# Optimization experiments

Hardware: AMD Instinct MI355X
Metric: run time of the kernel (lower is better)

## Reference

```python
import jax, jax.numpy as jnp
import numpy as np

N, D, H, B, K = 65536, 64, 128, 16, 16
EPS = 0.0

def setup_inputs() -> dict:
    key = jax.random.key(0)
    ks = jax.random.split(key, 5)
    x = jax.random.normal(ks[0], (N, D), dtype=jnp.float32)
    pos = jax.random.normal(ks[1], (N, 3), dtype=jnp.float32)
    batch = (jnp.arange(N, dtype=jnp.int32) // (N // B)).astype(jnp.int32)
    W1 = jax.random.normal(ks[2], (D, H), dtype=jnp.float32) * (1.0 / np.sqrt(D))
    b1 = jnp.zeros((H,), dtype=jnp.float32)
    W2 = jax.random.normal(ks[3], (H, D), dtype=jnp.float32) * (1.0 / np.sqrt(H))
    b2 = jnp.zeros((D,), dtype=jnp.float32)
    return {"x": x, "pos": pos, "batch": batch, "W1": W1, "b1": b1, "W2": W2, "b2": b2}

def reference(x, pos, batch, W1, b1, W2, b2):
    # batch is assumed contiguous with B equal segments of n nodes each
    n = N // B
    pos_s = pos.reshape(B, n, 3)
    x_s = x.reshape(B, n, D)
    # pairwise squared distances per segment via gram trick: [B, n, n]
    sq = jnp.sum(pos_s * pos_s, axis=-1)
    d2 = sq[:, :, None] + sq[:, None, :] - 2.0 * jnp.einsum('bic,bjc->bij', pos_s, pos_s)
    # exclude self-loops (loop=False in knn_graph)
    d2 = jnp.where(jnp.eye(n, dtype=bool)[None], jnp.inf, d2)
    # k nearest neighbors per node: indices [B, n, K]
    _, idx = jax.lax.top_k(-d2, K)
    # GIN sum aggregation: gather neighbor features and sum over K
    nb = x_s[jnp.arange(B)[:, None, None], idx]        # [B, n, K, D]
    agg = nb.sum(axis=2).reshape(N, D)                  # [N, D]
    h = (1.0 + EPS) * x + agg
    h = jax.nn.relu(h @ W1 + b1)
    out = h @ W2 + b2
    return out
```

## Files before the change

### kernel.cpp

```cpp
#include <hip/hip_runtime.h>
#include <math.h>

#define DIM  64
#define HID  128
#define KNN  16
#define SEG  1024
#define TSZ  128
#define CAP  14

typedef unsigned long long u64;
typedef __attribute__((ext_vector_type(8))) short short8;
typedef __attribute__((ext_vector_type(4))) float f32x4;
#define INF_BITS 0x7F800000u

__device__ __forceinline__ unsigned short bf16_rn(float f) {
    unsigned u = __float_as_uint(f);
    unsigned r = u + 0x7FFFu + ((u >> 16) & 1u);
    return (unsigned short)(r >> 16);
}
__device__ __forceinline__ float bf16_f32(unsigned short b) {
    return __uint_as_float(((unsigned)b) << 16);
}

__device__ __forceinline__ void ins16(float (&bd)[KNN], int (&bi)[KNN],
                                      float d, int g) {
    float cd = d; int ci = g;
    #pragma unroll
    for (int i = 0; i < KNN; ++i) {
        bool lt = cd < bd[i];
        float dl = lt ? cd : bd[i];
        float dh = lt ? bd[i] : cd;
        int   il = lt ? ci : bi[i];
        int   ih = lt ? bi[i] : ci;
        bd[i] = dl; bi[i] = il; cd = dh; ci = ih;
    }
}

__device__ __forceinline__ void drain_buf(const u64* bufe, int tid,
        float (&bd)[KNN], int (&bi)[KNN], int& cnt,
        unsigned* thrU, int l) {
    for (int t = 0; t < CAP; ++t) {
        if (__ballot(t < cnt) == 0ull) break;
        u64 e = bufe[t * 256 + tid];
        float d = __uint_as_float((unsigned)e);
        int   g = (int)(e >> 32);
        if ((t < cnt) && (d < bd[KNN - 1])) ins16(bd, bi, d, g);
    }
    cnt = 0;
    atomicMin(&thrU[l], __float_as_uint(bd[KNN - 1]));
}

struct f2 { float a, b; };
__device__ __forceinline__ f2 f2mul(f2 x, float s) {
    #pragma clang fp contract(off)
    f2 r; r.a = x.a * s; r.b = x.b * s; return r;
}
__device__ __forceinline__ f2 f2add(f2 x, f2 y) {
    #pragma clang fp contract(off)
    f2 r; r.a = x.a + y.a; r.b = x.b + y.b; return r;
}
__device__ __forceinline__ f2 f2adds(f2 x, float s) {
    #pragma clang fp contract(off)
    f2 r; r.a = s + x.a; r.b = s + x.b; return r;
}
__device__ __forceinline__ f2 f2sub(f2 x, f2 y) {
    #pragma clang fp contract(off)
    f2 r; r.a = x.a - y.a; r.b = x.b - y.b; return r;
}
__device__ __forceinline__ f2 d2pair(f2 Px, f2 Py, f2 Pz, f2 Ps,
                                     float qx, float qy, float qz, float qs) {
    f2 dot = f2add(f2add(f2mul(Px, qx), f2mul(Py, qy)), f2mul(Pz, qz));
    return f2sub(f2adds(Ps, qs), f2mul(dot, 2.0f));
}

template<bool CHECK>
__device__ __forceinline__ void knn_scan(
    const float* __restrict__ pos, int bbase, int segbase, int qlocal, int l,
    float qx, float qy, float qz, float qs,
    float* tx, float* ty, float* tz, float* ts,
    u64* bufe, unsigned* thrU, volatile unsigned* thrv, int tid,
    float (&bd)[KNN], int (&bi)[KNN])
{
    #pragma clang fp contract(off)
    int cnt = 0;

    #pragma unroll
    for (int m = 0; m < 2; ++m) {
        int t = (m << 6) + l;
        int g = (bbase + segbase + t) * 3;
        float ax = pos[g], ay = pos[g + 1], az = pos[g + 2];
        tx[t] = ax; ty[t] = ay; tz[t] = az;
        ts[t] = (ax * ax + ay * ay) + az * az;
    }

    __syncthreads();

    #pragma unroll
    for (int k = 0; k < KNN; ++k) { bd[k] = INFINITY; bi[k] = 0x7FFFFFFF; }
    for (int jj = 0; jj < KNN; ++jj) {
        float ax = tx[jj], ay = ty[jj], az = tz[jj], as = ts[jj];
        float dot = (ax * qx + ay * qy) + az * qz;
        float d2  = (qs + as) - 2.0f * dot;
        int cj = segbase + jj;
        if (cj == qlocal) d2 = INFINITY;
        ins16(bd, bi, d2, cj);
    }
    atomicMin(&thrU[l], __float_as_uint(bd[KNN - 1]));

    int jstart = KNN;
    for (int tb = 0; tb < SEG; tb += TSZ) {
        if (tb > 0) {
            #pragma unroll
            for (int m = 0; m < 2; ++m) {
                int t = (m << 6) + l;
                int g = (bbase + segbase + tb + t) * 3;
                float ax = pos[g], ay = pos[g + 1], az = pos[g + 2];
                tx[t] = ax; ty[t] = ay; tz[t] = az;
                ts[t] = (ax * ax + ay * ay) + az * az;
            }
        }
        for (int j = jstart; j < TSZ; j += 8) {
            float tl = __uint_as_float(thrv[l]);
            float4 X0 = *(const float4*)(tx + j);
            float4 X1 = *(const float4*)(tx + j + 4);
            float4 Y0 = *(const float4*)(ty + j);
            float4 Y1 = *(const float4*)(ty + j + 4);
            float4 Z0 = *(const float4*)(tz + j);
            float4 Z1 = *(const float4*)(tz + j + 4);
            float4 S0 = *(const float4*)(ts + j);
            float4 S1 = *(const float4*)(ts + j + 4);
            const int c0 = segbase + tb + j;

            f2 dA = d2pair({X0.x, X0.y}, {Y0.x, Y0.y}, {Z0.x, Z0.y}, {S0.x, S0.y},
                           qx, qy, qz, qs);
            f2 dB = d2pair({X0.z, X0.w}, {Y0.z, Y0.w}, {Z0.z, Z0.w}, {S0.z, S0.w},
                           qx, qy, qz, qs);
            f2 dC = d2pair({X1.x, X1.y}, {Y1.x, Y1.y}, {Z1.x, Z1.y}, {S1.x, S1.y},
                           qx, qy, qz, qs);
            f2 dD = d2pair({X1.z, X1.w}, {Y1.z, Y1.w}, {Z1.z, Z1.w}, {S1.z, S1.w},
                           qx, qy, qz, qs);
            if (CHECK) {
                int s = qlocal - c0;
                if (s == 0) dA.a = INFINITY;
                if (s == 1) dA.b = INFINITY;
                if (s == 2) dB.a = INFINITY;
                if (s == 3) dB.b = INFINITY;
                if (s == 4) dC.a = INFINITY;
                if (s == 5) dC.b = INFINITY;
                if (s == 6) dD.a = INFINITY;
                if (s == 7) dD.b = INFINITY;
            }

            if (dA.a <= tl) { bufe[cnt * 256 + tid] =
                ((u64)(unsigned)(c0 + 0) << 32) | __float_as_uint(dA.a); ++cnt; }
            if (dA.b <= tl) { bufe[cnt * 256 + tid] =
                ((u64)(unsigned)(c0 + 1) << 32) | __float_as_uint(dA.b); ++cnt; }
            if (dB.a <= tl) { bufe[cnt * 256 + tid] =
                ((u64)(unsigned)(c0 + 2) << 32) | __float_as_uint(dB.a); ++cnt; }
            if (dB.b <= tl) { bufe[cnt * 256 + tid] =
                ((u64)(unsigned)(c0 + 3) << 32) | __float_as_uint(dB.b); ++cnt; }
            if (dC.a <= tl) { bufe[cnt * 256 + tid] =
                ((u64)(unsigned)(c0 + 4) << 32) | __float_as_uint(dC.a); ++cnt; }
            if (dC.b <= tl) { bufe[cnt * 256 + tid] =
                ((u64)(unsigned)(c0 + 5) << 32) | __float_as_uint(dC.b); ++cnt; }
            if (dD.a <= tl) { bufe[cnt * 256 + tid] =
                ((u64)(unsigned)(c0 + 6) << 32) | __float_as_uint(dD.a); ++cnt; }
            if (dD.b <= tl) { bufe[cnt * 256 + tid] =
                ((u64)(unsigned)(c0 + 7) << 32) | __float_as_uint(dD.b); ++cnt; }

            if (__ballot(cnt >= CAP - 8) != 0ull)
                drain_buf(bufe, tid, bd, bi, cnt, thrU, l);
        }
        jstart = 0;
    }
    drain_buf(bufe, tid, bd, bi, cnt, thrU, l);
}

__global__ __launch_bounds__(256, 4) void knn_agg(
    const float* __restrict__ x, const float* __restrict__ pos,
    float* __restrict__ agg_out)
{
    __shared__ u64 smem[4640];

    const int tid = threadIdx.x;
    const int w   = tid >> 6;
    const int l   = tid & 63;

    const int qb     = blockIdx.x;
    const int batch  = qb >> 6;
    const int bbase  = batch << 12;
    const int qlocal = ((qb & 63) << 6) + l;
    const int qglob  = bbase + qlocal;

    float* tilef = (float*)smem;
    float* tx = tilef + w * 512;
    float* ty = tx + TSZ;
    float* tz = tx + 2 * TSZ;
    float* ts = tx + 3 * TSZ;
    unsigned* thrU = (unsigned*)(tilef + 2048);
    u64* bufe = smem + 1056;

    if (tid < 64) thrU[tid] = INF_BITS;

    float qx, qy, qz, qs;
    {
        #pragma clang fp contract(off)
        qx = pos[3 * qglob + 0];
        qy = pos[3 * qglob + 1];
        qz = pos[3 * qglob + 2];
        qs = (qx * qx + qy * qy) + qz * qz;
    }

    float bd[KNN]; int bi[KNN];
    const int segbase = w << 10;
    const int wself   = (qb & 63) >> 4;
    if (w == wself)
        knn_scan<true >(pos, bbase, segbase, qlocal, l, qx, qy, qz, qs,
                        tx, ty, tz, ts, bufe, thrU, thrU, tid, bd, bi);
    else
        knn_scan<false>(pos, bbase, segbase, qlocal, l, qx, qy, qz, qs,
                        tx, ty, tz, ts, bufe, thrU, thrU, tid, bd, bi);

    __syncthreads();

    float* md  = (float*)smem;
    int*  midx = (int*)(smem + 2048);
    #pragma unroll
    for (int k = 0; k < KNN; ++k) {
        int slot = (w << 4) + k;
        md[slot * 64 + l]   = bd[k];
        midx[slot * 64 + l] = bi[k];
    }
    __syncthreads();

    if (tid < 64) {
        float bd2[KNN]; int bi2[KNN];
        #pragma unroll
        for (int k = 0; k < KNN; ++k) {
            bd2[k] = md[k * 64 + tid];
            bi2[k] = midx[k * 64 + tid];
        }
        for (int c = KNN; c < 64; ++c) {
            float d = md[c * 64 + tid];
            int   g = midx[c * 64 + tid];
            if (d < bd2[KNN - 1]) ins16(bd2, bi2, d, g);
        }
        int* mi2 = (int*)smem;
        #pragma unroll
        for (int k = 0; k < KNN; ++k) mi2[k * 64 + tid] = bi2[k];
    }
    __syncthreads();

    {
        const int* mi2 = (const int*)smem;
        const int r  = tid >> 2;
        const int p  = tid & 3;
        const int q  = (qb << 6) + r;
        const int cb = p << 4;

        int idxs[KNN];
        #pragma unroll
        for (int k = 0; k < KNN; ++k) idxs[k] = mi2[k * 64 + r];

        float4 a0 = *(const float4*)(x + (size_t)q * DIM + cb + 0);
        float4 a1 = *(const float4*)(x + (size_t)q * DIM + cb + 4);
        float4 a2 = *(const float4*)(x + (size_t)q * DIM + cb + 8);
        float4 a3 = *(const float4*)(x + (size_t)q * DIM + cb + 12);

        #pragma unroll 4
        for (int k = 0; k < KNN; ++k) {
            const float* nr = x + (size_t)(bbase + idxs[k]) * DIM + cb;
            float4 v0 = *(const float4*)(nr + 0);
            float4 v1 = *(const float4*)(nr + 4);
            float4 v2 = *(const float4*)(nr + 8);
            float4 v3 = *(const float4*)(nr + 12);
            a0.x += v0.x; a0.y += v0.y; a0.z += v0.z; a0.w += v0.w;
            a1.x += v1.x; a1.y += v1.y; a1.z += v1.z; a1.w += v1.w;
            a2.x += v2.x; a2.y += v2.y; a2.z += v2.z; a2.w += v2.w;
            a3.x += v3.x; a3.y += v3.y; a3.z += v3.z; a3.w += v3.w;
        }

        float* o = agg_out + (size_t)q * DIM + cb;
        *(float4*)(o + 0)  = a0;
        *(float4*)(o + 4)  = a1;
        *(float4*)(o + 8)  = a2;
        *(float4*)(o + 12) = a3;
    }
}

__global__ void prep_bf16(const float* __restrict__ W1,
                          const float* __restrict__ W2,
                          unsigned short* __restrict__ ws) {
    int e = blockIdx.x * 256 + threadIdx.x;
    if (e < 8192) {
        int n = e >> 6, k = e & 63;
        float v = W1[k * HID + n];
        unsigned short h = bf16_rn(v);
        ws[e] = h;
        ws[8192 + e] = bf16_rn(v - bf16_f32(h));
    } else {
        int f = e - 8192;
        int n = f >> 7, k = f & 127;
        float v = W2[k * DIM + n];
        unsigned short h = bf16_rn(v);
        ws[16384 + f] = h;
        ws[24576 + f] = bf16_rn(v - bf16_f32(h));
    }
}

__global__ __launch_bounds__(256, 2) void mlp_mfma(
    const unsigned short* __restrict__ ws,
    const float* __restrict__ b1, const float* __restrict__ b2,
    float* __restrict__ io)
{
    __shared__ unsigned short hh[64 * 136];
    __shared__ unsigned short hl[64 * 136];

    const int tid  = threadIdx.x;
    const int w    = tid >> 6;
    const int lane = tid & 63;
    const int quad = lane >> 4;
    const int col  = lane & 15;
    const int rowbase = blockIdx.x * 64 + w * 16;

    const unsigned short* w1h = ws;
    const unsigned short* w1l = ws + 8192;
    const unsigned short* w2h = ws + 16384;
    const unsigned short* w2l = ws + 24576;

    short8 ah[2], al[2];
    #pragma unroll
    for (int ks = 0; ks < 2; ++ks) {
        const float* xr = io + (size_t)(rowbase + col) * DIM + ks * 32 + quad * 8;
        float4 v0 = *(const float4*)(xr);
        float4 v1 = *(const float4*)(xr + 4);
        float xv[8] = {v0.x, v0.y, v0.z, v0.w, v1.x, v1.y, v1.z, v1.w};
        #pragma unroll
        for (int j = 0; j < 8; ++j) {
            unsigned short hb = bf16_rn(xv[j]);
            ah[ks][j] = (short)hb;
            al[ks][j] = (short)bf16_rn(xv[j] - bf16_f32(hb));
        }
    }

    f32x4 acc1[8];
    #pragma unroll
    for (int t = 0; t < 8; ++t) acc1[t] = (f32x4){0.f, 0.f, 0.f, 0.f};

    #pragma unroll
    for (int t = 0; t < 8; ++t) {
        #pragma unroll
        for (int ks = 0; ks < 2; ++ks) {
            const int off = (t * 16 + col) * 64 + ks * 32 + quad * 8;
            short8 bh = *(const short8*)(w1h + off);
            short8 bl = *(const short8*)(w1l + off);
            acc1[t] = __builtin_amdgcn_mfma_f32_16x16x32_bf16(ah[ks], bh, acc1[t], 0, 0, 0);
            acc1[t] = __builtin_amdgcn_mfma_f32_16x16x32_bf16(al[ks], bh, acc1[t], 0, 0, 0);
            acc1[t] = __builtin_amdgcn_mfma_f32_16x16x32_bf16(ah[ks], bl, acc1[t], 0, 0, 0);
        }
    }

    #pragma unroll
    for (int t = 0; t < 8; ++t) {
        float bv = b1[t * 16 + col];
        #pragma unroll
        for (int r = 0; r < 4; ++r) {
            float h = fmaxf(acc1[t][r] + bv, 0.0f);
            unsigned short hb = bf16_rn(h);
            unsigned short lb = bf16_rn(h - bf16_f32(hb));
            int rowL = w * 16 + quad * 4 + r;
            hh[rowL * 136 + t * 16 + col] = hb;
            hl[rowL * 136 + t * 16 + col] = lb;
        }
    }
    __syncthreads();

    short8 a2h[4], a2l[4];
    #pragma unroll
    for (int ks = 0; ks < 4; ++ks) {
        const int off = (w * 16 + col) * 136 + ks * 32 + quad * 8;
        a2h[ks] = *(const short8*)(hh + off);
        a2l[ks] = *(const short8*)(hl + off);
    }

    f32x4 acc2[4];
    #pragma unroll
    for (int t = 0; t < 4; ++t) acc2[t] = (f32x4){0.f, 0.f, 0.f, 0.f};

    #pragma unroll
    for (int t = 0; t < 4; ++t) {
        #pragma unroll
        for (int ks = 0; ks < 4; ++ks) {
            const int off = (t * 16 + col) * 128 + ks * 32 + quad * 8;
            short8 bh = *(const short8*)(w2h + off);
            short8 bl = *(const short8*)(w2l + off);
            acc2[t] = __builtin_amdgcn_mfma_f32_16x16x32_bf16(a2h[ks], bh, acc2[t], 0, 0, 0);
            acc2[t] = __builtin_amdgcn_mfma_f32_16x16x32_bf16(a2l[ks], bh, acc2[t], 0, 0, 0);
            acc2[t] = __builtin_amdgcn_mfma_f32_16x16x32_bf16(a2h[ks], bl, acc2[t], 0, 0, 0);
        }
    }

    #pragma unroll
    for (int t = 0; t < 4; ++t) {
        float bv = b2[t * 16 + col];
        #pragma unroll
        for (int r = 0; r < 4; ++r) {
            io[(size_t)(rowbase + quad * 4 + r) * DIM + t * 16 + col] =
                acc2[t][r] + bv;
        }
    }
}

__global__ void prep_f32(const float* __restrict__ W1, float* __restrict__ w1t) {
    int e = blockIdx.x * 256 + threadIdx.x;
    int k = e >> 7, j = e & 127;
    w1t[j * 64 + k] = W1[e];
}

__global__ __launch_bounds__(256, 2) void mlp_valu(
    const float* __restrict__ w1t, const float* __restrict__ b1,
    const float* __restrict__ W2, const float* __restrict__ b2,
    float* __restrict__ io)
{
    __shared__ float hlds[128 * 65];
    const int tid  = threadIdx.x;
    const int r    = tid & 127;
    const int half = tid >> 7;
    const int row  = blockIdx.x * 128 + r;

    float xv[DIM];
    {
        const float4* xr = (const float4*)(io + (size_t)row * DIM);
        #pragma unroll
        for (int i = 0; i < 16; ++i) {
            float4 v = xr[i];
            xv[4*i] = v.x; xv[4*i+1] = v.y; xv[4*i+2] = v.z; xv[4*i+3] = v.w;
        }
    }
    float acc[DIM];
    #pragma unroll
    for (int c = 0; c < DIM; ++c) acc[c] = 0.0f;

    const int jb = half << 6;
    for (int jj = 0; jj < 64; ++jj) {
        const int j = jb + jj;
        const float* w1 = w1t + j * DIM;
        float s0 = 0.f, s1 = 0.f, s2 = 0.f, s3 = 0.f;
        #pragma unroll
        for (int c = 0; c < DIM; c += 4) {
            s0 = fmaf(w1[c + 0], xv[c + 0], s0);
            s1 = fmaf(w1[c + 1], xv[c + 1], s1);
            s2 = fmaf(w1[c + 2], xv[c + 2], s2);
            s3 = fmaf(w1[c + 3], xv[c + 3], s3);
        }
        float h = fmaxf((s0 + s1) + (s2 + s3) + b1[j], 0.0f);
        const float* w2 = W2 + j * DIM;
        #pragma unroll
        for (int c = 0; c < DIM; ++c) acc[c] = fmaf(h, w2[c], acc[c]);
    }

    if (half == 0) {
        #pragma unroll
        for (int c = 0; c < DIM; ++c) hlds[r * 65 + c] = acc[c];
    }
    __syncthreads();
    if (half == 1) {
        float* o = io + (size_t)row * DIM;
        #pragma unroll
        for (int c = 0; c < DIM; c += 4) {
            float4 r4;
            r4.x = acc[c + 0] + hlds[r * 65 + c + 0] + b2[c + 0];
            r4.y = acc[c + 1] + hlds[r * 65 + c + 1] + b2[c + 1];
            r4.z = acc[c + 2] + hlds[r * 65 + c + 2] + b2[c + 2];
            r4.w = acc[c + 3] + hlds[r * 65 + c + 3] + b2[c + 3];
            *(float4*)(o + c) = r4;
        }
    }
}

extern "C" void kernel_launch(void* const* d_in, const int* in_sizes, int n_in,
                              void* d_out, int out_size, void* d_ws, size_t ws_size,
                              hipStream_t stream) {
    (void)in_sizes; (void)n_in; (void)out_size;
    const float* x   = (const float*)d_in[0];
    const float* pos = (const float*)d_in[1];
    const float* W1  = (const float*)d_in[3];
    const float* b1  = (const float*)d_in[4];
    const float* W2  = (const float*)d_in[5];
    const float* b2  = (const float*)d_in[6];
    float* out = (float*)d_out;

    if (ws_size >= 65536) {
        prep_bf16<<<dim3(64), dim3(256), 0, stream>>>(W1, W2, (unsigned short*)d_ws);
        knn_agg<<<dim3(1024), dim3(256), 0, stream>>>(x, pos, out);
        mlp_mfma<<<dim3(1024), dim3(256), 0, stream>>>(
            (const unsigned short*)d_ws, b1, b2, out);
    } else {
        prep_f32<<<dim3(32), dim3(256), 0, stream>>>(W1, (float*)d_ws);
        knn_agg<<<dim3(1024), dim3(256), 0, stream>>>(x, pos, out);
        mlp_valu<<<dim3(512), dim3(256), 0, stream>>>(
            (const float*)d_ws, b1, W2, b2, out);
    }
}
```

Baseline: 357.6 us.

## Compute kNN distances with split-bf16 MFMA filtering and exact fp32 reselection

Replaces the per-thread VALU distance scan and per-lane top-16 insertion with MFMA-based distance tiles, using a hi/lo bf16 split to approximate the fp32 values. The approximate distances are filtered against a per-query threshold into shared-memory candidate lists. The lists are pruned periodically, and an exact fp32 recomputation then picks the final 16 neighbours. This trades the VALU-heavy dense scan for matrix-core throughput, at the cost of list-management atomics. There is a correctness risk if candidates overflow the list cap or fall outside the 0.01 slack margin. The fp32 MLP fallback path is also removed.

```diff
diff --git a/kernel.cpp b/kernel.cpp
--- a/kernel.cpp
+++ b/kernel.cpp
@@ -1,17 +1,17 @@
 #include <hip/hip_runtime.h>
 #include <math.h>
 
-#define DIM  64
-#define HID  128
-#define KNN  16
-#define SEG  1024
-#define TSZ  128
-#define CAP  14
+#define DIM    64
+#define HID    128
+#define KNN    16
+#define CHUNK  512
+#define LCAP   64
+#define LSTR   65
+#define EPS2   0.01f
 
 typedef unsigned long long u64;
 typedef __attribute__((ext_vector_type(8))) short short8;
 typedef __attribute__((ext_vector_type(4))) float f32x4;
-#define INF_BITS 0x7F800000u
 
 __device__ __forceinline__ unsigned short bf16_rn(float f) {
     unsigned u = __float_as_uint(f);
@@ -22,237 +22,216 @@
     return __uint_as_float(((unsigned)b) << 16);
 }
 
-__device__ __forceinline__ void ins16(float (&bd)[KNN], int (&bi)[KNN],
-                                      float d, int g) {
-    float cd = d; int ci = g;
-    #pragma unroll
-    for (int i = 0; i < KNN; ++i) {
-        bool lt = cd < bd[i];
-        float dl = lt ? cd : bd[i];
-        float dh = lt ? bd[i] : cd;
-        int   il = lt ? ci : bi[i];
-        int   ih = lt ? bi[i] : ci;
-        bd[i] = dl; bi[i] = il; cd = dh; ci = ih;
-    }
-}
-
-__device__ __forceinline__ void drain_buf(const u64* bufe, int tid,
-        float (&bd)[KNN], int (&bi)[KNN], int& cnt,
-        unsigned* thrU, int l) {
-    for (int t = 0; t < CAP; ++t) {
-        if (__ballot(t < cnt) == 0ull) break;
-        u64 e = bufe[t * 256 + tid];
-        float d = __uint_as_float((unsigned)e);
-        int   g = (int)(e >> 32);
-        if ((t < cnt) && (d < bd[KNN - 1])) ins16(bd, bi, d, g);
-    }
-    cnt = 0;
-    atomicMin(&thrU[l], __float_as_uint(bd[KNN - 1]));
-}
-
-struct f2 { float a, b; };
-__device__ __forceinline__ f2 f2mul(f2 x, float s) {
+__device__ __forceinline__ u64 pack_key(float d, unsigned idx) {
+    unsigned u = __float_as_uint(d);
+    unsigned m = u ^ ((unsigned)(((int)u) >> 31) | 0x80000000u);
+    return ((u64)m << 32) | idx;
+}
+
+__device__ __forceinline__ void ins16f(float (&b)[16], float d) {
+    float c = d;
+    #pragma unroll
+    for (int i = 0; i < 16; ++i) {
+        float lo = fminf(c, b[i]);
+        float hi = fmaxf(c, b[i]);
+        b[i] = lo; c = hi;
+    }
+}
+
+__device__ __forceinline__ void ins16k(u64 (&b)[16], u64 key) {
+    u64 c = key;
+    #pragma unroll
+    for (int i = 0; i < 16; ++i) {
+        bool lt = c < b[i];
+        u64 lo = lt ? c : b[i];
+        u64 hi = lt ? b[i] : c;
+        b[i] = lo; c = hi;
+    }
+}
+
+__device__ void exact_select(const float* __restrict__ pos, int bbase, int qloc,
+                             const u64* __restrict__ L, int n,
+                             int* __restrict__ out_idx, int qi) {
     #pragma clang fp contract(off)
-    f2 r; r.a = x.a * s; r.b = x.b * s; return r;
-}
-__device__ __forceinline__ f2 f2add(f2 x, f2 y) {
-    #pragma clang fp contract(off)
-    f2 r; r.a = x.a + y.a; r.b = x.b + y.b; return r;
-}
-__device__ __forceinline__ f2 f2adds(f2 x, float s) {
-    #pragma clang fp contract(off)
-    f2 r; r.a = s + x.a; r.b = s + x.b; return r;
-}
-__device__ __forceinline__ f2 f2sub(f2 x, f2 y) {
-    #pragma clang fp contract(off)
-    f2 r; r.a = x.a - y.a; r.b = x.b - y.b; return r;
-}
-__device__ __forceinline__ f2 d2pair(f2 Px, f2 Py, f2 Pz, f2 Ps,
-                                     float qx, float qy, float qz, float qs) {
-    f2 dot = f2add(f2add(f2mul(Px, qx), f2mul(Py, qy)), f2mul(Pz, qz));
-    return f2sub(f2adds(Ps, qs), f2mul(dot, 2.0f));
-}
-
-template<bool CHECK>
-__device__ __forceinline__ void knn_scan(
-    const float* __restrict__ pos, int bbase, int segbase, int qlocal, int l,
-    float qx, float qy, float qz, float qs,
-    float* tx, float* ty, float* tz, float* ts,
-    u64* bufe, unsigned* thrU, volatile unsigned* thrv, int tid,
-    float (&bd)[KNN], int (&bi)[KNN])
-{
-    #pragma clang fp contract(off)
-    int cnt = 0;
-
-    #pragma unroll
-    for (int m = 0; m < 2; ++m) {
-        int t = (m << 6) + l;
-        int g = (bbase + segbase + t) * 3;
-        float ax = pos[g], ay = pos[g + 1], az = pos[g + 2];
-        tx[t] = ax; ty[t] = ay; tz[t] = az;
-        ts[t] = (ax * ax + ay * ay) + az * az;
-    }
-
-    __syncthreads();
-
-    #pragma unroll
-    for (int k = 0; k < KNN; ++k) { bd[k] = INFINITY; bi[k] = 0x7FFFFFFF; }
-    for (int jj = 0; jj < KNN; ++jj) {
-        float ax = tx[jj], ay = ty[jj], az = tz[jj], as = ts[jj];
-        float dot = (ax * qx + ay * qy) + az * qz;
-        float d2  = (qs + as) - 2.0f * dot;
-        int cj = segbase + jj;
-        if (cj == qlocal) d2 = INFINITY;
-        ins16(bd, bi, d2, cj);
-    }
-    atomicMin(&thrU[l], __float_as_uint(bd[KNN - 1]));
-
-    int jstart = KNN;
-    for (int tb = 0; tb < SEG; tb += TSZ) {
-        if (tb > 0) {
-            #pragma unroll
-            for (int m = 0; m < 2; ++m) {
-                int t = (m << 6) + l;
-                int g = (bbase + segbase + tb + t) * 3;
-                float ax = pos[g], ay = pos[g + 1], az = pos[g + 2];
-                tx[t] = ax; ty[t] = ay; tz[t] = az;
-                ts[t] = (ax * ax + ay * ay) + az * az;
-            }
-        }
-        for (int j = jstart; j < TSZ; j += 8) {
-            float tl = __uint_as_float(thrv[l]);
-            float4 X0 = *(const float4*)(tx + j);
-            float4 X1 = *(const float4*)(tx + j + 4);
-            float4 Y0 = *(const float4*)(ty + j);
-            float4 Y1 = *(const float4*)(ty + j + 4);
-            float4 Z0 = *(const float4*)(tz + j);
-            float4 Z1 = *(const float4*)(tz + j + 4);
-            float4 S0 = *(const float4*)(ts + j);
-            float4 S1 = *(const float4*)(ts + j + 4);
-            const int c0 = segbase + tb + j;
-
-            f2 dA = d2pair({X0.x, X0.y}, {Y0.x, Y0.y}, {Z0.x, Z0.y}, {S0.x, S0.y},
-                           qx, qy, qz, qs);
-            f2 dB = d2pair({X0.z, X0.w}, {Y0.z, Y0.w}, {Z0.z, Z0.w}, {S0.z, S0.w},
-                           qx, qy, qz, qs);
-            f2 dC = d2pair({X1.x, X1.y}, {Y1.x, Y1.y}, {Z1.x, Z1.y}, {S1.x, S1.y},
-                           qx, qy, qz, qs);
-            f2 dD = d2pair({X1.z, X1.w}, {Y1.z, Y1.w}, {Z1.z, Z1.w}, {S1.z, S1.w},
-                           qx, qy, qz, qs);
-            if (CHECK) {
-                int s = qlocal - c0;
-                if (s == 0) dA.a = INFINITY;
-                if (s == 1) dA.b = INFINITY;
-                if (s == 2) dB.a = INFINITY;
-                if (s == 3) dB.b = INFINITY;
-                if (s == 4) dC.a = INFINITY;
-                if (s == 5) dC.b = INFINITY;
-                if (s == 6) dD.a = INFINITY;
-                if (s == 7) dD.b = INFINITY;
-            }
-
-            if (dA.a <= tl) { bufe[cnt * 256 + tid] =
-                ((u64)(unsigned)(c0 + 0) << 32) | __float_as_uint(dA.a); ++cnt; }
-            if (dA.b <= tl) { bufe[cnt * 256 + tid] =
-                ((u64)(unsigned)(c0 + 1) << 32) | __float_as_uint(dA.b); ++cnt; }
-            if (dB.a <= tl) { bufe[cnt * 256 + tid] =
-                ((u64)(unsigned)(c0 + 2) << 32) | __float_as_uint(dB.a); ++cnt; }
-            if (dB.b <= tl) { bufe[cnt * 256 + tid] =
-                ((u64)(unsigned)(c0 + 3) << 32) | __float_as_uint(dB.b); ++cnt; }
-            if (dC.a <= tl) { bufe[cnt * 256 + tid] =
-                ((u64)(unsigned)(c0 + 4) << 32) | __float_as_uint(dC.a); ++cnt; }
-            if (dC.b <= tl) { bufe[cnt * 256 + tid] =
-                ((u64)(unsigned)(c0 + 5) << 32) | __float_as_uint(dC.b); ++cnt; }
-            if (dD.a <= tl) { bufe[cnt * 256 + tid] =
-                ((u64)(unsigned)(c0 + 6) << 32) | __float_as_uint(dD.a); ++cnt; }
-            if (dD.b <= tl) { bufe[cnt * 256 + tid] =
-                ((u64)(unsigned)(c0 + 7) << 32) | __float_as_uint(dD.b); ++cnt; }
-
-            if (__ballot(cnt >= CAP - 8) != 0ull)
-                drain_buf(bufe, tid, bd, bi, cnt, thrU, l);
-        }
-        jstart = 0;
-    }
-    drain_buf(bufe, tid, bd, bi, cnt, thrU, l);
-}
-
-__global__ __launch_bounds__(256, 4) void knn_agg(
+    const float* pq = pos + (size_t)(bbase + qloc) * 3;
+    float qx = pq[0], qy = pq[1], qz = pq[2];
+    float qs = (qx * qx + qy * qy) + qz * qz;
+    u64 b[16];
+    #pragma unroll
+    for (int k = 0; k < 16; ++k) b[k] = 0xFFFFFFFFFFFFFFFFull;
+    for (int i = 0; i < n; ++i) {
+        unsigned c = (unsigned)(L[i] & 0xFFFFFFFFull);
+        const float* pc = pos + (size_t)(bbase + (int)c) * 3;
+        float ax = pc[0], ay = pc[1], az = pc[2];
+        float dot = (qx * ax + qy * ay) + qz * az;
+        float as_ = (ax * ax + ay * ay) + az * az;
+        float d2  = (qs + as_) - 2.0f * dot;
+        u64 key = pack_key(d2, c);
+        if (key < b[15]) ins16k(b, key);
+    }
+    #pragma unroll
+    for (int k = 0; k < 16; ++k)
+        out_idx[k * 64 + qi] = (int)(b[k] & 0xFFFFFFFFull);
+}
+
+__global__ __launch_bounds__(256, 3) void knn_mfma(
     const float* __restrict__ x, const float* __restrict__ pos,
     float* __restrict__ agg_out)
 {
-    __shared__ u64 smem[4640];
-
-    const int tid = threadIdx.x;
-    const int w   = tid >> 6;
-    const int l   = tid & 63;
-
-    const int qb     = blockIdx.x;
-    const int batch  = qb >> 6;
-    const int bbase  = batch << 12;
-    const int qlocal = ((qb & 63) << 6) + l;
-    const int qglob  = bbase + qlocal;
-
-    float* tilef = (float*)smem;
-    float* tx = tilef + w * 512;
-    float* ty = tx + TSZ;
-    float* tz = tx + 2 * TSZ;
-    float* ts = tx + 3 * TSZ;
-    unsigned* thrU = (unsigned*)(tilef + 2048);
-    u64* bufe = smem + 1056;
-
-    if (tid < 64) thrU[tid] = INF_BITS;
-
-    float qx, qy, qz, qs;
+    __shared__ u64 smem[6274];
+    unsigned short* bh = (unsigned short*)smem;
+    unsigned short* bl = bh + CHUNK * 8;
+    u64*   lists = smem + 2048;
+    unsigned* cntA = (unsigned*)(smem + 6208);
+    float* thrF = (float*)(smem + 6240);
+    unsigned short* zeroPack = (unsigned short*)(smem + 6272);
+
+    const int tid  = threadIdx.x;
+    const int w    = tid >> 6;
+    const int lane = tid & 63;
+    const int quad = lane >> 4;
+    const int col  = lane & 15;
+
+    const int qb    = blockIdx.x;
+    const int bbase = (qb >> 6) << 12;
+    const int qrow0 = (qb & 63) << 6;
+
+    if (tid < 64) { cntA[tid] = 0u; thrF[tid] = INFINITY; }
+    if (tid < 8)  zeroPack[tid] = 0;
+
+    short8 ah = (short8)0, al = (short8)0;
+    if (quad == 0) {
+        const float* pq = pos + (size_t)(bbase + qrow0 + w * 16 + col) * 3;
+        float qx = pq[0], qy = pq[1], qz = pq[2];
+        float qs = (qx * qx + qy * qy) + qz * qz;
+        float v[8] = {qx, qy, qz, qs, 1.0f, 0.f, 0.f, 0.f};
+        #pragma unroll
+        for (int j = 0; j < 8; ++j) {
+            unsigned short hb = bf16_rn(v[j]);
+            ah[j] = (short)hb;
+            al[j] = (short)bf16_rn(v[j] - bf16_f32(hb));
+        }
+    }
+
+    float t0 = INFINITY, t1 = INFINITY, t2 = INFINITY, t3 = INFINITY;
+
+    for (int chunk = 0; chunk < 8; ++chunk) {
+        __syncthreads();
+        for (int e = tid; e < CHUNK; e += 256) {
+            const float* pc = pos + (size_t)(bbase + (chunk << 9) + e) * 3;
+            float cx = pc[0], cy = pc[1], cz = pc[2];
+            float cs = (cx * cx + cy * cy) + cz * cz;
+            float v[8] = {-2.f * cx, -2.f * cy, -2.f * cz, 1.0f, cs, 0.f, 0.f, 0.f};
+            short8 hi, lo;
+            #pragma unroll
+            for (int j = 0; j < 8; ++j) {
+                unsigned short hb = bf16_rn(v[j]);
+                hi[j] = (short)hb;
+                lo[j] = (short)bf16_rn(v[j] - bf16_f32(hb));
+            }
+            *(short8*)(bh + e * 8) = hi;
+            *(short8*)(bl + e * 8) = lo;
+        }
+        __syncthreads();
+
+        for (int t = 0; t < 32; ++t) {
+            const int coff = ((t << 4) + col) << 3;
+            const unsigned short* ph = (quad == 0) ? (bh + coff) : zeroPack;
+            const unsigned short* pl = (quad == 0) ? (bl + coff) : zeroPack;
+            short8 vbh = *(const short8*)ph;
+            short8 vbl = *(const short8*)pl;
+
+            f32x4 acc = (f32x4){0.f, 0.f, 0.f, 0.f};
+            acc = __builtin_amdgcn_mfma_f32_16x16x32_bf16(ah, vbh, acc, 0, 0, 0);
+            acc = __builtin_amdgcn_mfma_f32_16x16x32_bf16(al, vbh, acc, 0, 0, 0);
+            acc = __builtin_amdgcn_mfma_f32_16x16x32_bf16(ah, vbl, acc, 0, 0, 0);
+
+            bool p = (acc[0] <= t0) | (acc[1] <= t1) | (acc[2] <= t2) | (acc[3] <= t3);
+            if (__ballot(p) != 0ull) {
+                const int cl = (chunk << 9) + (t << 4) + col;
+                const int qbase = (w << 4) + (quad << 2);
+                if (acc[0] <= t0) {
+                    int qi = qbase + 0;
+                    if (cl != qrow0 + qi) {
+                        unsigned pp = atomicAdd(&cntA[qi], 1u);
+                        if (pp < (unsigned)LCAP)
+                            lists[qi * LSTR + pp] =
+                                ((u64)__float_as_uint(acc[0]) << 32) | (unsigned)cl;
+                    }
+                }
+                if (acc[1] <= t1) {
+                    int qi = qbase + 1;
+                    if (cl != qrow0 + qi) {
+                        unsigned pp = atomicAdd(&cntA[qi], 1u);
+                        if (pp < (unsigned)LCAP)
+                            lists[qi * LSTR + pp] =
+                                ((u64)__float_as_uint(acc[1]) << 32) | (unsigned)cl;
+                    }
+                }
+                if (acc[2] <= t2) {
+                    int qi = qbase + 2;
+                    if (cl != qrow0 + qi) {
+                        unsigned pp = atomicAdd(&cntA[qi], 1u);
+                        if (pp < (unsigned)LCAP)
+                            lists[qi * LSTR + pp] =
+                                ((u64)__float_as_uint(acc[2]) << 32) | (unsigned)cl;
+                    }
+                }
+                if (acc[3] <= t3) {
+                    int qi = qbase + 3;
+                    if (cl != qrow0 + qi) {
+                        unsigned pp = atomicAdd(&cntA[qi], 1u);
+                        if (pp < (unsigned)LCAP)
+                            lists[qi * LSTR + pp] =
+                                ((u64)__float_as_uint(acc[3]) << 32) | (unsigned)cl;
+                    }
+                }
+            }
+
+            unsigned cother = cntA[(w << 4) + col];
+            bool trig  = (lane < 16) && (cother >= (unsigned)(LCAP - 16));
+            bool force = (chunk == 0) && (t == 1);
+            if (force || (__ballot(trig) != 0ull)) {
+                if (lane < 16) {
+                    int qi = (w << 4) + lane;
+                    int n = (int)min(cntA[qi], (unsigned)LCAP);
+                    float b16[16];
+                    #pragma unroll
+                    for (int k = 0; k < 16; ++k) b16[k] = INFINITY;
+                    u64* L = lists + qi * LSTR;
+                    for (int i = 0; i < n; ++i) {
+                        float d = __uint_as_float((unsigned)(L[i] >> 32));
+                        if (d < b16[15]) ins16f(b16, d);
+                    }
+                    float keep = b16[15] + EPS2;
+                    int m2 = 0;
+                    for (int i = 0; i < n; ++i) {
+                        u64 e = L[i];
+                        if (__uint_as_float((unsigned)(e >> 32)) <= keep) {
+                            L[m2] = e; ++m2;
+                        }
+                    }
+                    cntA[qi] = (unsigned)m2;
+                    thrF[qi] = keep;
+                }
+                const int qb4 = (w << 4) + (quad << 2);
+                t0 = thrF[qb4 + 0]; t1 = thrF[qb4 + 1];
+                t2 = thrF[qb4 + 2]; t3 = thrF[qb4 + 3];
+            }
+        }
+    }
+
+    __syncthreads();
+
+    int* mi2 = (int*)smem;
+    if (lane < 16) {
+        int qi = (w << 4) + lane;
+        int n = (int)min(cntA[qi], (unsigned)LCAP);
+        exact_select(pos, bbase, qrow0 + qi, lists + qi * LSTR, n, mi2, qi);
+    }
+    __syncthreads();
+
     {
-        #pragma clang fp contract(off)
-        qx = pos[3 * qglob + 0];
-        qy = pos[3 * qglob + 1];
-        qz = pos[3 * qglob + 2];
-        qs = (qx * qx + qy * qy) + qz * qz;
-    }
-
-    float bd[KNN]; int bi[KNN];
-    const int segbase = w << 10;
-    const int wself   = (qb & 63) >> 4;
-    if (w == wself)
-        knn_scan<true >(pos, bbase, segbase, qlocal, l, qx, qy, qz, qs,
-                        tx, ty, tz, ts, bufe, thrU, thrU, tid, bd, bi);
-    else
-        knn_scan<false>(pos, bbase, segbase, qlocal, l, qx, qy, qz, qs,
-                        tx, ty, tz, ts, bufe, thrU, thrU, tid, bd, bi);
-
-    __syncthreads();
-
-    float* md  = (float*)smem;
-    int*  midx = (int*)(smem + 2048);
-    #pragma unroll
-    for (int k = 0; k < KNN; ++k) {
-        int slot = (w << 4) + k;
-        md[slot * 64 + l]   = bd[k];
-        midx[slot * 64 + l] = bi[k];
-    }
-    __syncthreads();
-
-    if (tid < 64) {
-        float bd2[KNN]; int bi2[KNN];
-        #pragma unroll
-        for (int k = 0; k < KNN; ++k) {
-            bd2[k] = md[k * 64 + tid];
-            bi2[k] = midx[k * 64 + tid];
-        }
-        for (int c = KNN; c < 64; ++c) {
-            float d = md[c * 64 + tid];
-            int   g = midx[c * 64 + tid];
-            if (d < bd2[KNN - 1]) ins16(bd2, bi2, d, g);
-        }
-        int* mi2 = (int*)smem;
-        #pragma unroll
-        for (int k = 0; k < KNN; ++k) mi2[k * 64 + tid] = bi2[k];
-    }
-    __syncthreads();
-
-    {
-        const int* mi2 = (const int*)smem;
         const int r  = tid >> 2;
         const int p  = tid & 3;
         const int q  = (qb << 6) + r;
@@ -411,77 +390,10 @@
     }
 }
 
-__global__ void prep_f32(const float* __restrict__ W1, float* __restrict__ w1t) {
-    int e = blockIdx.x * 256 + threadIdx.x;
-    int k = e >> 7, j = e & 127;
-    w1t[j * 64 + k] = W1[e];
-}
-
-__global__ __launch_bounds__(256, 2) void mlp_valu(
-    const float* __restrict__ w1t, const float* __restrict__ b1,
-    const float* __restrict__ W2, const float* __restrict__ b2,
-    float* __restrict__ io)
-{
-    __shared__ float hlds[128 * 65];
-    const int tid  = threadIdx.x;
-    const int r    = tid & 127;
-    const int half = tid >> 7;
-    const int row  = blockIdx.x * 128 + r;
-
-    float xv[DIM];
-    {
-        const float4* xr = (const float4*)(io + (size_t)row * DIM);
-        #pragma unroll
-        for (int i = 0; i < 16; ++i) {
-            float4 v = xr[i];
-            xv[4*i] = v.x; xv[4*i+1] = v.y; xv[4*i+2] = v.z; xv[4*i+3] = v.w;
-        }
-    }
-    float acc[DIM];
-    #pragma unroll
-    for (int c = 0; c < DIM; ++c) acc[c] = 0.0f;
-
-    const int jb = half << 6;
-    for (int jj = 0; jj < 64; ++jj) {
-        const int j = jb + jj;
-        const float* w1 = w1t + j * DIM;
-        float s0 = 0.f, s1 = 0.f, s2 = 0.f, s3 = 0.f;
-        #pragma unroll
-        for (int c = 0; c < DIM; c += 4) {
-            s0 = fmaf(w1[c + 0], xv[c + 0], s0);
-            s1 = fmaf(w1[c + 1], xv[c + 1], s1);
-            s2 = fmaf(w1[c + 2], xv[c + 2], s2);
-            s3 = fmaf(w1[c + 3], xv[c + 3], s3);
-        }
-        float h = fmaxf((s0 + s1) + (s2 + s3) + b1[j], 0.0f);
-        const float* w2 = W2 + j * DIM;
-        #pragma unroll
-        for (int c = 0; c < DIM; ++c) acc[c] = fmaf(h, w2[c], acc[c]);
-    }
-
-    if (half == 0) {
-        #pragma unroll
-        for (int c = 0; c < DIM; ++c) hlds[r * 65 + c] = acc[c];
-    }
-    __syncthreads();
-    if (half == 1) {
-        float* o = io + (size_t)row * DIM;
-        #pragma unroll
-        for (int c = 0; c < DIM; c += 4) {
-            float4 r4;
-            r4.x = acc[c + 0] + hlds[r * 65 + c + 0] + b2[c + 0];
-            r4.y = acc[c + 1] + hlds[r * 65 + c + 1] + b2[c + 1];
-            r4.z = acc[c + 2] + hlds[r * 65 + c + 2] + b2[c + 2];
-            r4.w = acc[c + 3] + hlds[r * 65 + c + 3] + b2[c + 3];
-            *(float4*)(o + c) = r4;
-        }
-    }
-}
-
 extern "C" void kernel_launch(void* const* d_in, const int* in_sizes, int n_in,
                               void* d_out, int out_size, void* d_ws, size_t ws_size,
                               hipStream_t stream) {
-    (void)in_sizes; (void)n_in; (void)out_size;
+    (void)in_sizes; (void)n_in; (void)out_size; (void)ws_size;
     const float* x   = (const float*)d_in[0];
     const float* pos = (const float*)d_in[1];
     const float* W1  = (const float*)d_in[3];
@@ -490,15 +402,8 @@
     const float* b2  = (const float*)d_in[6];
     float* out = (float*)d_out;
 
-    if (ws_size >= 65536) {
-        prep_bf16<<<dim3(64), dim3(256), 0, stream>>>(W1, W2, (unsigned short*)d_ws);
-        knn_agg<<<dim3(1024), dim3(256), 0, stream>>>(x, pos, out);
-        mlp_mfma<<<dim3(1024), dim3(256), 0, stream>>>(
-            (const unsigned short*)d_ws, b1, b2, out);
-    } else {
-        prep_f32<<<dim3(32), dim3(256), 0, stream>>>(W1, (float*)d_ws);
-        knn_agg<<<dim3(1024), dim3(256), 0, stream>>>(x, pos, out);
-        mlp_valu<<<dim3(512), dim3(256), 0, stream>>>(
-            (const float*)d_ws, b1, W2, b2, out);
-    }
-}
+    prep_bf16<<<dim3(64), dim3(256), 0, stream>>>(W1, W2, (unsigned short*)d_ws);
+    knn_mfma<<<dim3(1024), dim3(256), 0, stream>>>(x, pos, out);
+    mlp_mfma<<<dim3(1024), dim3(256), 0, stream>>>(
+        (const unsigned short*)d_ws, b1, b2, out);
+}
```

Measured after the change: 654.0 us. 82.9% more time.
